# Kernel optimization log

Hardware: AMD Instinct MI355X
Metric: run time of the kernel (lower is better)

The kernel has to match this reference:

```python
import jax, jax.numpy as jnp
import numpy as np

IT = 31          # input (feed-forward) taps
FB = 15          # decision-feedback taps
HID = 32         # hidden nodes
ALPHA = 4.0      # compressed-sigmoid alpha
BETA = 0.5       # compressed-sigmoid beta
LEVELS = jnp.array([-3.0, -1.0, 1.0, 3.0], dtype=jnp.float32)  # PAM-4 levels
B, T = 512, 32768


def setup_inputs() -> dict:
    key = jax.random.key(0)
    k_x, k_w1, k_b1, k_w2, k_b2 = jax.random.split(key, 5)
    x = jax.random.normal(k_x, (B, T), dtype=jnp.float32)
    W1 = jax.random.normal(k_w1, (IT + FB, HID), dtype=jnp.float32) * (1.0 / np.sqrt(IT + FB))
    b1 = jax.random.normal(k_b1, (HID,), dtype=jnp.float32) * 0.1
    W2 = jax.random.normal(k_w2, (HID,), dtype=jnp.float32) * (1.0 / np.sqrt(HID))
    b2 = jax.random.normal(k_b2, (1,), dtype=jnp.float32) * 0.1
    return {"x": x, "W1": W1, "b1": b1, "W2": W2, "b2": b2}


def reference(x, W1, b1, W2, b2):
    # Inference-mode forward (labels=None): decision-feedback recurrence.
    Bb, Tt = x.shape
    # Left-pad so step i sees x[:, i-IT+1 : i+1] with zero padding at the start,
    # exactly matching the torch slicing + zero-pad logic.
    xp = jnp.pad(x, ((0, 0), (IT - 1, 0)))

    def step(buf, i):
        win = jax.lax.dynamic_slice(xp, (0, i), (Bb, IT))      # (B, IT)
        comb = jnp.concatenate([win, buf], axis=1)             # (B, IT+FB)
        h = jnp.tanh(comb @ W1 + b1)                           # (B, HID)
        y = h @ W2 + b2[0]                                     # (B,)
        # PAM-4 hard decision
        idx = jnp.argmin(jnp.abs(y[:, None] - LEVELS), axis=-1)
        y_hat = LEVELS[idx]
        gamma = 1.0 - jnp.abs(y - y_hat)
        # compressed sigmoid: 0.5*((1-e^{-v})/(1+e^{-v}) + 1) == sigmoid(v)
        s = jax.nn.sigmoid(ALPHA * (gamma / BETA - 1.0))
        y_tilde = s * y_hat + (1.0 - s) * y
        # roll feedback buffer by 1 and insert newest decision at position 0
        new_buf = jnp.concatenate([y_tilde[:, None], buf[:, :-1]], axis=1)
        return new_buf, y

    buf0 = jnp.zeros((Bb, FB), dtype=x.dtype)
    _, ys = jax.lax.scan(step, buf0, jnp.arange(Tt))           # ys: (T, B)
    return ys.T                                                 # (B, T)
```

## Files before the change

kernel.cpp:

```cpp
#include <hip/hip_runtime.h>
#include <type_traits>

constexpr int IT_ = 31;
constexpr int FB_ = 15;
constexpr int HID_ = 32;
constexpr int T_LEN = 32768;
constexpr int NSEG = 8;
constexpr int WARM = 1024;
constexpr int SEGLEN = (T_LEN - WARM) / NSEG;
constexpr int SEG0LEN = SEGLEN + WARM;
constexpr float K2LOG2E = 2.8853900817779268f;
constexpr float KS1 = 11.541560327111708f;
constexpr float KS0 = -5.770780163555854f;

static_assert(SEG0LEN % 32 == 0 && SEGLEN % 32 == 0 && WARM % 32 == 0, "chunk align");
static_assert(SEG0LEN + (NSEG - 1) * SEGLEN == T_LEN, "coverage");

template<int N, typename F>
__device__ __forceinline__ void static_for(F&& f) {
  if constexpr (N > 0) {
    static_for<N - 1>(f);
    f(std::integral_constant<int, N - 1>{});
  }
}

template<int CTRL>
__device__ __forceinline__ float dpp_add(float v) {
  int d = __builtin_amdgcn_update_dpp(0, __float_as_int(v), CTRL, 0xf, 0xf, false);
  return v + __int_as_float(d);
}

template<int OFF>
__device__ __forceinline__ float swz(float v) {
  return __int_as_float(__builtin_amdgcn_ds_swizzle(__float_as_int(v), OFF));
}

__device__ __forceinline__ float exp2_raw(float x) {
#if __has_builtin(__builtin_amdgcn_exp2f)
  return __builtin_amdgcn_exp2f(x);
#else
  float r;
  asm("v_exp_f32 %0, %1" : "=v"(r) : "v"(x));
  return r;
#endif
}

__device__ __forceinline__ float cross_row16_add(float v) {
#if __has_builtin(__builtin_amdgcn_permlane16_swap)
  typedef int v2i __attribute__((ext_vector_type(2)));
  v2i pr = __builtin_amdgcn_permlane16_swap(__float_as_int(v), __float_as_int(v),
                                            false, false);
  return __int_as_float(pr.x) + __int_as_float(pr.y);
#else
  float u;
  float t = v;
  asm("v_mov_b32 %0, %1\n\t"
      "v_permlane16_swap_b32 %0, %1"
      : "=&v"(u), "+v"(t));
  return u + t;
#endif
}

__global__ __launch_bounds__(64)
__attribute__((amdgpu_waves_per_eu(2, 2)))
void wdrnn_eq_kernel(const float* __restrict__ x,
                     const float* __restrict__ W1,
                     const float* __restrict__ b1,
                     const float* __restrict__ W2,
                     const float* __restrict__ b2,
                     float* __restrict__ out) {
  const int lane = threadIdx.x;
  const int j = lane & 31;
  const int half = lane >> 5;
  const int batch = blockIdx.x * 2 + half;
  const int seg = blockIdx.y;
  const int t0 = (seg == 0) ? 0 : (SEG0LEN + (seg - 1) * SEGLEN);
  const int tw = (seg == 0) ? 0 : (t0 - WARM);
  const int tend = t0 + ((seg == 0) ? SEG0LEN : SEGLEN);

  float w[IT_ + FB_];
  #pragma unroll
  for (int q = 0; q < IT_ + FB_; ++q) w[q] = W1[q * HID_ + j] * K2LOG2E;
  const float b1v = b1[j] * K2LOG2E;
  const float w2v = W2[j];
  const float b2v = b2[0];
  const float wfb0 = w[IT_];
  const float mslope = -2.0f * w2v;
  const float mbase  = w2v + b2v * (1.0f / 32.0f);

  const float* xrow = x + (size_t)batch * T_LEN;
  float* orow = out + (size_t)batch * T_LEN;

  float xwin[62];
  float br[16];
  #pragma unroll
  for (int i = 0; i < 30; ++i) {
    const int idx = tw - 30 + i;
    xwin[i] = (idx >= 0) ? xrow[idx] : 0.0f;
  }
  #pragma unroll
  for (int i = 30; i < 62; ++i) xwin[i] = 0.0f;
  #pragma unroll
  for (int i = 0; i < 16; ++i) br[i] = 0.0f;

  float cur = xrow[tw + j];

  for (int tb = tw; tb < tend; tb += 32) {
    const int nidx = (tb + 32 < T_LEN) ? (tb + 32 + j) : (T_LEN - 1);
    float nxt = xrow[nidx];

    static_for<32>([&](auto Ic) {
      constexpr int I = Ic.value;
      xwin[30 + I] = swz<(I << 5)>(cur);
    });

    float ystage = 0.0f;
    static_for<32>([&](auto Uc) {
      constexpr int U = Uc.value;

      float a0 = b1v, a1 = 0.f, a2 = 0.f, a3 = 0.f;
      static_for<IT_>([&](auto Kc) {
        constexpr int K = Kc.value;
        const float xv = xwin[30 + U - K];
        const float wv = w[IT_ - 1 - K];
        if constexpr ((K & 3) == 0)      a0 = fmaf(xv, wv, a0);
        else if constexpr ((K & 3) == 1) a1 = fmaf(xv, wv, a1);
        else if constexpr ((K & 3) == 2) a2 = fmaf(xv, wv, a2);
        else                             a3 = fmaf(xv, wv, a3);
      });
      static_for<FB_ - 1>([&](auto Fc) {
        constexpr int F = Fc.value + 1;
        const float bv = br[(U + 31 - F) & 15];
        const float wv = w[IT_ + F];
        if constexpr ((F & 3) == 0)      a0 = fmaf(bv, wv, a0);
        else if constexpr ((F & 3) == 1) a1 = fmaf(bv, wv, a1);
        else if constexpr ((F & 3) == 2) a2 = fmaf(bv, wv, a2);
        else                             a3 = fmaf(bv, wv, a3);
      });
      float rest = (a0 + a1) + (a2 + a3);

      float acc = fmaf(br[(U + 15) & 15], wfb0, rest);
      float e2a = exp2_raw(acc);
      float r = __builtin_amdgcn_rcpf(e2a + 1.0f);
      float yv = fmaf(r, mslope, mbase);

      yv = dpp_add<0xB1>(yv);
      yv = dpp_add<0x4E>(yv);
      yv = dpp_add<0x124>(yv);
      yv = dpp_add<0x128>(yv);
      float y = cross_row16_add(yv);

      float c = ceilf(y * 0.5f);
      float yhat = __builtin_amdgcn_fmed3f(fmaf(2.0f, c, -1.0f), -3.0f, 3.0f);
      float d = yhat - y;
      float e = exp2_raw(fmaf(KS1, fabsf(d), KS0));
      float s = __builtin_amdgcn_rcpf(1.0f + e);
      float yt = fmaf(s, d, y);

      br[U & 15] = yt;
      ystage = (j == U) ? y : ystage;
    });

    if (tb >= t0) orow[tb + j] = ystage;
    cur = nxt;

    #pragma unroll
    for (int i = 0; i < 30; ++i) xwin[i] = xwin[i + 32];
  }
}

extern "C" void kernel_launch(void* const* d_in, const int* in_sizes, int n_in,
                              void* d_out, int out_size, void* d_ws, size_t ws_size,
                              hipStream_t stream) {
  (void)n_in; (void)out_size; (void)d_ws; (void)ws_size;
  const float* x  = (const float*)d_in[0];
  const float* W1 = (const float*)d_in[1];
  const float* b1 = (const float*)d_in[2];
  const float* W2 = (const float*)d_in[3];
  const float* b2 = (const float*)d_in[4];
  float* out = (float*)d_out;

  const int B = in_sizes[0] / T_LEN;
  const int blocks = B / 2;

  hipLaunchKernelGGL(wdrnn_eq_kernel, dim3(blocks, NSEG), dim3(64), 0, stream,
                     x, W1, b1, W2, b2, out);
}
```

Before: 1.226 ms.

## Process two batch rows per half-wave using packed f32x2 FMAs

Each 32-lane half-wave now runs the recurrence for two batch rows at once. Values are held as two-wide float vectors so the dot-product FMAs can lower to packed FMA instructions, which covers two rows per instruction and gives two independent dependency chains to interleave. Block count halves and occupancy is set to one wave per EU, since the doubled window and weight registers raise register pressure. The scalar transcendental and DPP steps are duplicated, and fewer waves means less latency hiding between waves.

```diff
diff --git a/kernel.cpp b/kernel.cpp
--- a/kernel.cpp
+++ b/kernel.cpp
@@ -1,5 +1,7 @@
 #include <hip/hip_runtime.h>
 #include <type_traits>
+
+typedef float f32x2 __attribute__((ext_vector_type(2)));
 
 constexpr int IT_ = 31;
 constexpr int FB_ = 15;
@@ -24,10 +26,18 @@
   }
 }
 
+__device__ __forceinline__ f32x2 make2(float s) { return f32x2{s, s}; }
+
+__device__ __forceinline__ f32x2 pk_fma(f32x2 a, f32x2 b, f32x2 c) {
+  return __builtin_elementwise_fma(a, b, c);
+}
+
 template<int CTRL>
-__device__ __forceinline__ float dpp_add(float v) {
-  int d = __builtin_amdgcn_update_dpp(0, __float_as_int(v), CTRL, 0xf, 0xf, false);
-  return v + __int_as_float(d);
+__device__ __forceinline__ f32x2 dpp_add2(f32x2 v) {
+  f32x2 d;
+  d.x = __int_as_float(__builtin_amdgcn_update_dpp(0, __float_as_int(v.x), CTRL, 0xf, 0xf, false));
+  d.y = __int_as_float(__builtin_amdgcn_update_dpp(0, __float_as_int(v.y), CTRL, 0xf, 0xf, false));
+  return v + d;
 }
 
 template<int OFF>
@@ -62,7 +72,7 @@
 }
 
 __global__ __launch_bounds__(64)
-__attribute__((amdgpu_waves_per_eu(2, 2)))
+__attribute__((amdgpu_waves_per_eu(1, 1)))
 void wdrnn_eq_kernel(const float* __restrict__ x,
                      const float* __restrict__ W1,
                      const float* __restrict__ b1,
@@ -72,96 +82,132 @@
   const int lane = threadIdx.x;
   const int j = lane & 31;
   const int half = lane >> 5;
-  const int batch = blockIdx.x * 2 + half;
+  const int base = blockIdx.x * 4 + half * 2;
   const int seg = blockIdx.y;
   const int t0 = (seg == 0) ? 0 : (SEG0LEN + (seg - 1) * SEGLEN);
   const int tw = (seg == 0) ? 0 : (t0 - WARM);
   const int tend = t0 + ((seg == 0) ? SEG0LEN : SEGLEN);
 
-  float w[IT_ + FB_];
-  #pragma unroll
-  for (int q = 0; q < IT_ + FB_; ++q) w[q] = W1[q * HID_ + j] * K2LOG2E;
-  const float b1v = b1[j] * K2LOG2E;
+  f32x2 w2[IT_ + FB_];
+  #pragma unroll
+  for (int q = 0; q < IT_ + FB_; ++q) w2[q] = make2(W1[q * HID_ + j] * K2LOG2E);
+  const f32x2 b1v2 = make2(b1[j] * K2LOG2E);
   const float w2v = W2[j];
   const float b2v = b2[0];
-  const float wfb0 = w[IT_];
-  const float mslope = -2.0f * w2v;
-  const float mbase  = w2v + b2v * (1.0f / 32.0f);
-
-  const float* xrow = x + (size_t)batch * T_LEN;
-  float* orow = out + (size_t)batch * T_LEN;
-
-  float xwin[62];
-  float br[16];
+  const f32x2 wfb02   = w2[IT_];
+  const f32x2 mslope2 = make2(-2.0f * w2v);
+  const f32x2 mbase2  = make2(w2v + b2v * (1.0f / 32.0f));
+  const f32x2 k2      = make2(2.0f);
+  const f32x2 km1     = make2(-1.0f);
+  const f32x2 khalf   = make2(0.5f);
+  const f32x2 kone    = make2(1.0f);
+  const f32x2 ks1v    = make2(KS1);
+  const f32x2 ks0v    = make2(KS0);
+
+  const float* xrow0 = x + (size_t)base * T_LEN;
+  const float* xrow1 = x + (size_t)(base + 1) * T_LEN;
+  float* orow0 = out + (size_t)base * T_LEN;
+  float* orow1 = out + (size_t)(base + 1) * T_LEN;
+
+  f32x2 xwin[62];
+  f32x2 br[16];
   #pragma unroll
   for (int i = 0; i < 30; ++i) {
     const int idx = tw - 30 + i;
-    xwin[i] = (idx >= 0) ? xrow[idx] : 0.0f;
+    xwin[i] = (idx >= 0) ? f32x2{xrow0[idx], xrow1[idx]} : make2(0.0f);
   }
   #pragma unroll
-  for (int i = 30; i < 62; ++i) xwin[i] = 0.0f;
-  #pragma unroll
-  for (int i = 0; i < 16; ++i) br[i] = 0.0f;
-
-  float cur = xrow[tw + j];
+  for (int i = 30; i < 62; ++i) xwin[i] = make2(0.0f);
+  #pragma unroll
+  for (int i = 0; i < 16; ++i) br[i] = make2(0.0f);
+
+  f32x2 cur = {xrow0[tw + j], xrow1[tw + j]};
 
   for (int tb = tw; tb < tend; tb += 32) {
     const int nidx = (tb + 32 < T_LEN) ? (tb + 32 + j) : (T_LEN - 1);
-    float nxt = xrow[nidx];
+    f32x2 nxt = {xrow0[nidx], xrow1[nidx]};
 
     static_for<32>([&](auto Ic) {
       constexpr int I = Ic.value;
-      xwin[30 + I] = swz<(I << 5)>(cur);
+      f32x2 t;
+      t.x = swz<(I << 5)>(cur.x);
+      t.y = swz<(I << 5)>(cur.y);
+      xwin[30 + I] = t;
     });
 
-    float ystage = 0.0f;
+    f32x2 ystage = make2(0.0f);
     static_for<32>([&](auto Uc) {
       constexpr int U = Uc.value;
 
-      float a0 = b1v, a1 = 0.f, a2 = 0.f, a3 = 0.f;
+      f32x2 a0 = b1v2, a1 = make2(0.f), a2 = make2(0.f), a3 = make2(0.f);
       static_for<IT_>([&](auto Kc) {
         constexpr int K = Kc.value;
-        const float xv = xwin[30 + U - K];
-        const float wv = w[IT_ - 1 - K];
-        if constexpr ((K & 3) == 0)      a0 = fmaf(xv, wv, a0);
-        else if constexpr ((K & 3) == 1) a1 = fmaf(xv, wv, a1);
-        else if constexpr ((K & 3) == 2) a2 = fmaf(xv, wv, a2);
-        else                             a3 = fmaf(xv, wv, a3);
+        const f32x2 xv = xwin[30 + U - K];
+        const f32x2 wv = w2[IT_ - 1 - K];
+        if constexpr ((K & 3) == 0)      a0 = pk_fma(xv, wv, a0);
+        else if constexpr ((K & 3) == 1) a1 = pk_fma(xv, wv, a1);
+        else if constexpr ((K & 3) == 2) a2 = pk_fma(xv, wv, a2);
+        else                             a3 = pk_fma(xv, wv, a3);
       });
       static_for<FB_ - 1>([&](auto Fc) {
         constexpr int F = Fc.value + 1;
-        const float bv = br[(U + 31 - F) & 15];
-        const float wv = w[IT_ + F];
-        if constexpr ((F & 3) == 0)      a0 = fmaf(bv, wv, a0);
-        else if constexpr ((F & 3) == 1) a1 = fmaf(bv, wv, a1);
-        else if constexpr ((F & 3) == 2) a2 = fmaf(bv, wv, a2);
-        else                             a3 = fmaf(bv, wv, a3);
+        const f32x2 bv = br[(U + 31 - F) & 15];
+        const f32x2 wv = w2[IT_ + F];
+        if constexpr ((F & 3) == 0)      a0 = pk_fma(bv, wv, a0);
+        else if constexpr ((F & 3) == 1) a1 = pk_fma(bv, wv, a1);
+        else if constexpr ((F & 3) == 2) a2 = pk_fma(bv, wv, a2);
+        else                             a3 = pk_fma(bv, wv, a3);
       });
-      float rest = (a0 + a1) + (a2 + a3);
-
-      float acc = fmaf(br[(U + 15) & 15], wfb0, rest);
-      float e2a = exp2_raw(acc);
-      float r = __builtin_amdgcn_rcpf(e2a + 1.0f);
-      float yv = fmaf(r, mslope, mbase);
-
-      yv = dpp_add<0xB1>(yv);
-      yv = dpp_add<0x4E>(yv);
-      yv = dpp_add<0x124>(yv);
-      yv = dpp_add<0x128>(yv);
-      float y = cross_row16_add(yv);
-
-      float c = ceilf(y * 0.5f);
-      float yhat = __builtin_amdgcn_fmed3f(fmaf(2.0f, c, -1.0f), -3.0f, 3.0f);
-      float d = yhat - y;
-      float e = exp2_raw(fmaf(KS1, fabsf(d), KS0));
-      float s = __builtin_amdgcn_rcpf(1.0f + e);
-      float yt = fmaf(s, d, y);
+      f32x2 rest = (a0 + a1) + (a2 + a3);
+
+      f32x2 acc = pk_fma(br[(U + 15) & 15], wfb02, rest);
+      f32x2 e2a;
+      e2a.x = exp2_raw(acc.x);
+      e2a.y = exp2_raw(acc.y);
+      f32x2 ep = e2a + kone;
+      f32x2 r;
+      r.x = __builtin_amdgcn_rcpf(ep.x);
+      r.y = __builtin_amdgcn_rcpf(ep.y);
+      f32x2 yv = pk_fma(r, mslope2, mbase2);
+
+      yv = dpp_add2<0xB1>(yv);
+      yv = dpp_add2<0x4E>(yv);
+      yv = dpp_add2<0x124>(yv);
+      yv = dpp_add2<0x128>(yv);
+      f32x2 y2;
+      y2.x = cross_row16_add(yv.x);
+      y2.y = cross_row16_add(yv.y);
+
+      f32x2 h2 = y2 * khalf;
+      f32x2 c2;
+      c2.x = ceilf(h2.x);
+      c2.y = ceilf(h2.y);
+      f32x2 l2 = pk_fma(k2, c2, km1);
+      f32x2 yhat;
+      yhat.x = __builtin_amdgcn_fmed3f(l2.x, -3.0f, 3.0f);
+      yhat.y = __builtin_amdgcn_fmed3f(l2.y, -3.0f, 3.0f);
+      f32x2 d2 = yhat - y2;
+      f32x2 ad;
+      ad.x = fabsf(d2.x);
+      ad.y = fabsf(d2.y);
+      f32x2 earg = pk_fma(ks1v, ad, ks0v);
+      f32x2 e2;
+      e2.x = exp2_raw(earg.x);
+      e2.y = exp2_raw(earg.y);
+      f32x2 den = e2 + kone;
+      f32x2 s2;
+      s2.x = __builtin_amdgcn_rcpf(den.x);
+      s2.y = __builtin_amdgcn_rcpf(den.y);
+      f32x2 yt = pk_fma(s2, d2, y2);
 
       br[U & 15] = yt;
-      ystage = (j == U) ? y : ystage;
+      if (j == U) ystage = y2;
     });
 
-    if (tb >= t0) orow[tb + j] = ystage;
+    if (tb >= t0) {
+      orow0[tb + j] = ystage.x;
+      orow1[tb + j] = ystage.y;
+    }
     cur = nxt;
 
     #pragma unroll
@@ -181,7 +227,7 @@
   float* out = (float*)d_out;
 
   const int B = in_sizes[0] / T_LEN;
-  const int blocks = B / 2;
+  const int blocks = B / 4;
 
   hipLaunchKernelGGL(wdrnn_eq_kernel, dim3(blocks, NSEG), dim3(64), 0, stream,
                      x, W1, b1, W2, b2, out);
```

New measurement: 1.155 ms. -5.7%, faster.
